# Optimization experiments

Hardware: AMD Instinct MI355X
Metric: run time of the kernel (lower is better)

## Reference

```python
import jax, jax.numpy as jnp
import numpy as np
from functools import partial

ALPHA = 0.1
THETA = 0.5
N_NODES = 100000
N_EDGES = 3200000


def _gcn_norm(edge_index, num_nodes):
    # add self loops, compute symmetric normalization D^-1/2 (A+I) D^-1/2
    loops = jnp.arange(num_nodes, dtype=edge_index.dtype)
    src = jnp.concatenate([edge_index[0], loops])
    dst = jnp.concatenate([edge_index[1], loops])
    deg = jax.ops.segment_sum(jnp.ones_like(dst, dtype=jnp.float32), dst,
                              num_segments=num_nodes)
    dinv = jnp.where(deg > 0, jax.lax.rsqrt(deg), 0.0)
    norm = dinv[src] * dinv[dst]  # [E+N]
    return src, dst, norm


def _propagate(h, src, dst, norm, num_nodes):
    # out[i] = sum_{e: dst[e]=i} norm[e] * h[src[e]]
    msg = h[src] * norm[:, None]
    return jax.ops.segment_sum(msg, dst, num_segments=num_nodes)


def setup_inputs() -> dict:
    key = jax.random.key(0)
    ks = jax.random.split(key, 7)
    H, Fin, Fout, L = 256, 512, 64, 8
    x = jax.random.normal(ks[0], (N_NODES, Fin), dtype=jnp.float32)
    edge_index = jax.random.randint(ks[1], (2, N_EDGES), 0, N_NODES, dtype=jnp.int64)
    s = 1.0 / np.sqrt(Fin)
    W0 = jax.random.normal(ks[2], (Fin, H), dtype=jnp.float32) * s
    b0 = jax.random.normal(ks[3], (H,), dtype=jnp.float32) * 0.01
    Ws = jax.random.normal(ks[4], (L, H, H), dtype=jnp.float32) / np.sqrt(H)
    Wc = jax.random.normal(ks[5], (H, Fout), dtype=jnp.float32) / np.sqrt(H)
    bc = jax.random.normal(ks[6], (Fout,), dtype=jnp.float32) * 0.01
    return {"x": x, "edge_index": edge_index, "W0": W0, "b0": b0,
            "Ws": Ws, "Wc": Wc, "bc": bc}


def reference(x, edge_index, W0, b0, Ws, Wc, bc):
    num_nodes = x.shape[0]
    src, dst, norm = _gcn_norm(edge_index, num_nodes)
    # initial projection (dropout is identity in eval mode)
    x0 = jax.nn.relu(x @ W0 + b0)  # [N, H]
    h = x0
    layer_num = Ws.shape[0]
    for i in range(layer_num):
        beta = float(np.log(THETA / (i + 1) + 1.0))
        agg = _propagate(h, src, dst, norm, num_nodes)          # Ahat @ h
        z = (1.0 - ALPHA) * agg + ALPHA * x0                    # initial residual
        h = jax.nn.relu((1.0 - beta) * z + beta * (z @ Ws[i]))  # identity mapping
    embedding = h
    logits = embedding @ Wc + bc
    soft_label = jax.nn.softmax(logits, axis=1)
    hard_label = jnp.argmax(soft_label, axis=1)
    return logits, embedding, soft_label, hard_label
```

## Files before the change

### kernel.cpp

```cpp
#include <hip/hip_runtime.h>
#include <hip/hip_bf16.h>
#include <math.h>

#define NN   100000
#define FIN  512
#define HH   256
#define FOUT 64

typedef __attribute__((ext_vector_type(8))) short s16x8;
typedef __attribute__((ext_vector_type(4))) float f32x4;

__global__ void k_count(const int* __restrict__ dst, int* __restrict__ cnt, int E) {
    int i = blockIdx.x * 256 + threadIdx.x;
    if (i < E) atomicAdd(&cnt[dst[i]], 1);
}

__global__ void k_block_sums(const int* __restrict__ cnt, int* __restrict__ partial, int n) {
    __shared__ int red[256];
    int base = blockIdx.x * 1024;
    int t = threadIdx.x;
    int s = 0;
#pragma unroll
    for (int i = 0; i < 4; i++) { int idx = base + t * 4 + i; if (idx < n) s += cnt[idx]; }
    red[t] = s; __syncthreads();
    for (int off = 128; off > 0; off >>= 1) {
        if (t < off) red[t] += red[t + off];
        __syncthreads();
    }
    if (t == 0) partial[blockIdx.x] = red[0];
}

__global__ void k_scan_partials(int* partial, int nb, int* row_ptr, int n) {
    if (threadIdx.x == 0) {
        int run = 0;
        for (int i = 0; i < nb; i++) { int v = partial[i]; partial[i] = run; run += v; }
        row_ptr[n] = run;
    }
}

__global__ void k_write_rowptr(const int* __restrict__ cnt, const int* __restrict__ partial,
                               int* __restrict__ row_ptr, int* __restrict__ cur, int n) {
    __shared__ int sc[256];
    int base = blockIdx.x * 1024;
    int t = threadIdx.x;
    int v[4]; int s = 0;
#pragma unroll
    for (int i = 0; i < 4; i++) { int idx = base + t * 4 + i; v[i] = (idx < n) ? cnt[idx] : 0; s += v[i]; }
    sc[t] = s; __syncthreads();
    for (int off = 1; off < 256; off <<= 1) {
        int add = (t >= off) ? sc[t - off] : 0;
        __syncthreads();
        sc[t] += add;
        __syncthreads();
    }
    int run = partial[blockIdx.x] + sc[t] - s;
#pragma unroll
    for (int i = 0; i < 4; i++) {
        int idx = base + t * 4 + i;
        if (idx < n) { row_ptr[idx] = run; cur[idx] = run; run += v[i]; }
    }
}

__global__ void k_dinv(const int* __restrict__ cnt, float* __restrict__ dinv, int n) {
    int i = blockIdx.x * 256 + threadIdx.x;
    if (i < n) dinv[i] = 1.0f / sqrtf((float)(cnt[i] + 1));
}

__global__ void k_scatter(const int* __restrict__ src, const int* __restrict__ dst,
                          const float* __restrict__ dinv, int* __restrict__ cur,
                          int* __restrict__ src_sorted, float* __restrict__ norm_sorted, int E) {
    int i = blockIdx.x * 256 + threadIdx.x;
    if (i < E) {
        int s = src[i], d = dst[i];
        int p = atomicAdd(&cur[d], 1);
        src_sorted[p] = s;
        norm_sorted[p] = dinv[s] * dinv[d];
    }
}

__device__ __forceinline__ short f2bf_rn(float f) {
    unsigned b = __float_as_uint(f);
    unsigned r = b + 0x7FFFu + ((b >> 16) & 1u);
    return (short)(r >> 16);
}
__device__ __forceinline__ float bf2f(short h) {
    return __uint_as_float(((unsigned)(unsigned short)h) << 16);
}
__device__ __forceinline__ void split_bf16(float f, short& hi, short& lo) {
    hi = f2bf_rn(f);
    lo = f2bf_rn(f - bf2f(hi));
}

__global__ void k_wprep(const float* __restrict__ W, short* __restrict__ whi,
                        short* __restrict__ wlo, int K) {
    int t = blockIdx.x * 256 + threadIdx.x;
    int total = K * HH / 8;
    if (t >= total) return;
    int colin = t & 15, g = (t >> 4) & 3, nt = (t >> 6) & 15, kt = t >> 10;
    int col = nt * 16 + colin, kb = kt * 32 + g * 8;
    s16x8 h8, l8;
#pragma unroll
    for (int j = 0; j < 8; j++) {
        float f = W[(size_t)(kb + j) * HH + col];
        short h, l; split_bf16(f, h, l);
        h8[j] = h; l8[j] = l;
    }
    *(s16x8*)&whi[(size_t)t * 8] = h8;
    *(s16x8*)&wlo[(size_t)t * 8] = l8;
}

__global__ __launch_bounds__(256) void k_gemm0(
    const float* __restrict__ A, const short* __restrict__ Whi, const short* __restrict__ Wlo,
    const float* __restrict__ bias, float* __restrict__ C, int M) {
    __shared__ short As_hi[2048];
    __shared__ short As_lo[2048];
    int tid = threadIdx.x, lane = tid & 63, wid = tid >> 6;
    int wm = wid >> 1, wn = wid & 1;
    int bm = blockIdx.x * 64;
    int st_row = tid >> 2, st_g = tid & 3;
    int st_cphys = ((st_row & 15) ^ ((st_g & 1) << 2)) + 16 * st_g + 64 * (st_row >> 4);
    const float* st_ap = A + (size_t)(bm + st_row) * FIN + st_g * 8;
    bool st_ok = (bm + st_row) < M;
    int fr_g = lane >> 4, fr_r = lane & 15;
    int fr_base = (fr_r ^ ((fr_g & 1) << 2)) + 16 * fr_g;
    int c0 = (fr_base + 64 * (wm * 2 + 0)) * 8;
    int c1 = (fr_base + 64 * (wm * 2 + 1)) * 8;
    int lane_off = fr_g * 16 + fr_r;
    f32x4 acc[2][8] = {};
    for (int kt = 0; kt < FIN / 32; kt++) {
        int k0 = kt * 32;
        f32x4 v0 = {0.f, 0.f, 0.f, 0.f}, v1 = {0.f, 0.f, 0.f, 0.f};
        if (st_ok) { v0 = *(const f32x4*)(st_ap + k0); v1 = *(const f32x4*)(st_ap + k0 + 4); }
        s16x8 h8, l8;
        {
            float fv[8] = {v0.x, v0.y, v0.z, v0.w, v1.x, v1.y, v1.z, v1.w};
#pragma unroll
            for (int j = 0; j < 8; j++) { short hh, ll; split_bf16(fv[j], hh, ll); h8[j] = hh; l8[j] = ll; }
        }
        *(s16x8*)&As_hi[st_cphys * 8] = h8;
        *(s16x8*)&As_lo[st_cphys * 8] = l8;
        __syncthreads();
        s16x8 ah0 = *(const s16x8*)&As_hi[c0], al0 = *(const s16x8*)&As_lo[c0];
        s16x8 ah1 = *(const s16x8*)&As_hi[c1], al1 = *(const s16x8*)&As_lo[c1];
        size_t btile = (size_t)kt * 1024 + (size_t)(wn * 8) * 64;
#pragma unroll
        for (int ct = 0; ct < 8; ct++) {
            s16x8 bh = *(const s16x8*)&Whi[(btile + ct * 64 + lane_off) * 8];
            s16x8 bl = *(const s16x8*)&Wlo[(btile + ct * 64 + lane_off) * 8];
            acc[0][ct] = __builtin_amdgcn_mfma_f32_16x16x32_bf16(ah0, bh, acc[0][ct], 0, 0, 0);
            acc[0][ct] = __builtin_amdgcn_mfma_f32_16x16x32_bf16(al0, bh, acc[0][ct], 0, 0, 0);
            acc[0][ct] = __builtin_amdgcn_mfma_f32_16x16x32_bf16(ah0, bl, acc[0][ct], 0, 0, 0);
            acc[1][ct] = __builtin_amdgcn_mfma_f32_16x16x32_bf16(ah1, bh, acc[1][ct], 0, 0, 0);
            acc[1][ct] = __builtin_amdgcn_mfma_f32_16x16x32_bf16(al1, bh, acc[1][ct], 0, 0, 0);
            acc[1][ct] = __builtin_amdgcn_mfma_f32_16x16x32_bf16(ah1, bl, acc[1][ct], 0, 0, 0);
        }
        __syncthreads();
    }
    int rsub = (lane >> 4) * 4, csub = lane & 15;
#pragma unroll
    for (int rt = 0; rt < 2; rt++)
#pragma unroll
        for (int ct = 0; ct < 8; ct++) {
            int col = wn * 128 + ct * 16 + csub;
            int r0 = bm + wm * 32 + rt * 16 + rsub;
#pragma unroll
            for (int reg = 0; reg < 4; reg++) {
                int row = r0 + reg;
                if (row < M) C[(size_t)row * HH + col] = fmaxf(acc[rt][ct][reg] + bias[col], 0.f);
            }
        }
}

__global__ __launch_bounds__(256) void k_layer(
    const float* __restrict__ h, const float* __restrict__ x0,
    const int* __restrict__ row_ptr, const int* __restrict__ src_sorted,
    const float* __restrict__ norm_sorted, const float* __restrict__ dinv,
    const short* __restrict__ Whi, const short* __restrict__ Wlo,
    float* __restrict__ C, int M, float beta) {
    __shared__ float zbuf[16384];
    __shared__ short As_hi[2048];
    __shared__ short As_lo[2048];
    int tid = threadIdx.x, lane = tid & 63, wid = tid >> 6;
    int bm = blockIdx.x * 64;

    {
        int f = lane * 4;
        for (int r16 = 0; r16 < 16; r16++) {
            int rl = r16 * 4 + wid;
            int node = bm + rl;
            if (node < M) {
                size_t base = (size_t)node * HH + f;
                float di = dinv[node];
                float sw = di * di;
                f32x4 acc = *(const f32x4*)&h[base];
                acc *= sw;
                int e = __builtin_amdgcn_readfirstlane(row_ptr[node]);
                int end = __builtin_amdgcn_readfirstlane(row_ptr[node + 1]);
                for (; e + 3 < end; e += 4) {
                    int s0 = src_sorted[e], s1 = src_sorted[e + 1];
                    int s2 = src_sorted[e + 2], s3 = src_sorted[e + 3];
                    float w0 = norm_sorted[e], w1 = norm_sorted[e + 1];
                    float w2 = norm_sorted[e + 2], w3 = norm_sorted[e + 3];
                    f32x4 v0 = *(const f32x4*)&h[(size_t)s0 * HH + f];
                    f32x4 v1 = *(const f32x4*)&h[(size_t)s1 * HH + f];
                    f32x4 v2 = *(const f32x4*)&h[(size_t)s2 * HH + f];
                    f32x4 v3 = *(const f32x4*)&h[(size_t)s3 * HH + f];
                    acc += w0 * v0 + w1 * v1 + w2 * v2 + w3 * v3;
                }
                for (; e < end; e++) {
                    int s0 = src_sorted[e];
                    float w0 = norm_sorted[e];
                    acc += w0 * (*(const f32x4*)&h[(size_t)s0 * HH + f]);
                }
                f32x4 xv = __builtin_nontemporal_load((const f32x4*)&x0[base]);
                f32x4 z = 0.9f * acc + 0.1f * xv;
                int phys = lane ^ (rl & 7);
                *(f32x4*)&zbuf[rl * 256 + phys * 4] = z;
            }
        }
    }
    __syncthreads();

    int wm = wid >> 1, wn = wid & 1;
    int st_row = tid >> 2, st_g = tid & 3;
    int st_cphys = ((st_row & 15) ^ ((st_g & 1) << 2)) + 16 * st_g + 64 * (st_row >> 4);
    int fr_g = lane >> 4, fr_r = lane & 15;
    int fr_base = (fr_r ^ ((fr_g & 1) << 2)) + 16 * fr_g;
    int c0 = (fr_base + 64 * (wm * 2 + 0)) * 8;
    int c1 = (fr_base + 64 * (wm * 2 + 1)) * 8;
    int lane_off = fr_g * 16 + fr_r;
    int zr = st_row * 256, swz = st_row & 7;
    f32x4 acc[2][8] = {};
    for (int kt = 0; kt < 8; kt++) {
        int b0 = kt * 8 + st_g * 2;
        f32x4 v0 = *(const f32x4*)&zbuf[zr + ((b0 ^ swz) * 4)];
        f32x4 v1 = *(const f32x4*)&zbuf[zr + (((b0 + 1) ^ swz) * 4)];
        s16x8 h8, l8;
        {
            float fv[8] = {v0.x, v0.y, v0.z, v0.w, v1.x, v1.y, v1.z, v1.w};
#pragma unroll
            for (int j = 0; j < 8; j++) { short hh, ll; split_bf16(fv[j], hh, ll); h8[j] = hh; l8[j] = ll; }
        }
        *(s16x8*)&As_hi[st_cphys * 8] = h8;
        *(s16x8*)&As_lo[st_cphys * 8] = l8;
        __syncthreads();
        s16x8 ah0 = *(const s16x8*)&As_hi[c0], al0 = *(const s16x8*)&As_lo[c0];
        s16x8 ah1 = *(const s16x8*)&As_hi[c1], al1 = *(const s16x8*)&As_lo[c1];
        size_t btile = (size_t)kt * 1024 + (size_t)(wn * 8) * 64;
#pragma unroll
        for (int ct = 0; ct < 8; ct++) {
            s16x8 bh = *(const s16x8*)&Whi[(btile + ct * 64 + lane_off) * 8];
            s16x8 bl = *(const s16x8*)&Wlo[(btile + ct * 64 + lane_off) * 8];
            acc[0][ct] = __builtin_amdgcn_mfma_f32_16x16x32_bf16(ah0, bh, acc[0][ct], 0, 0, 0);
            acc[0][ct] = __builtin_amdgcn_mfma_f32_16x16x32_bf16(al0, bh, acc[0][ct], 0, 0, 0);
            acc[0][ct] = __builtin_amdgcn_mfma_f32_16x16x32_bf16(ah0, bl, acc[0][ct], 0, 0, 0);
            acc[1][ct] = __builtin_amdgcn_mfma_f32_16x16x32_bf16(ah1, bh, acc[1][ct], 0, 0, 0);
            acc[1][ct] = __builtin_amdgcn_mfma_f32_16x16x32_bf16(al1, bh, acc[1][ct], 0, 0, 0);
            acc[1][ct] = __builtin_amdgcn_mfma_f32_16x16x32_bf16(ah1, bl, acc[1][ct], 0, 0, 0);
        }
        __syncthreads();
    }

    int rsub = (lane >> 4) * 4, csub = lane & 15;
    float ob = 1.f - beta;
#pragma unroll
    for (int rt = 0; rt < 2; rt++)
#pragma unroll
        for (int ct = 0; ct < 8; ct++) {
            int col = wn * 128 + ct * 16 + csub;
            int r0 = wm * 32 + rt * 16 + rsub;
#pragma unroll
            for (int reg = 0; reg < 4; reg++) {
                int rl = r0 + reg;
                int row = bm + rl;
                if (row < M) {
                    float z = zbuf[rl * 256 + (((col >> 2) ^ (rl & 7)) * 4) + (col & 3)];
                    C[(size_t)row * HH + col] = fmaxf(ob * z + beta * acc[rt][ct][reg], 0.f);
                }
            }
        }
}

__global__ __launch_bounds__(256) void k_final(
    const float* __restrict__ h, const float* __restrict__ Wc, const float* __restrict__ bc,
    float* __restrict__ logits, float* __restrict__ soft, float* __restrict__ hard) {
    int wv = threadIdx.x >> 6, lane = threadIdx.x & 63;
    int node = blockIdx.x * 4 + wv;
    if (node >= NN) return;
    const float* hr = &h[(size_t)node * HH];
    float acc = bc[lane];
    for (int k = 0; k < HH; k += 4) {
        f32x4 hv = *(const f32x4*)&hr[k];
        acc += hv.x * Wc[(k + 0) * FOUT + lane];
        acc += hv.y * Wc[(k + 1) * FOUT + lane];
        acc += hv.z * Wc[(k + 2) * FOUT + lane];
        acc += hv.w * Wc[(k + 3) * FOUT + lane];
    }
    float m = acc;
    for (int off = 32; off > 0; off >>= 1) m = fmaxf(m, __shfl_xor(m, off));
    float ev = expf(acc - m);
    float s = ev;
    for (int off = 32; off > 0; off >>= 1) s += __shfl_xor(s, off);
    float sm = ev / s;
    int idx = lane; float v = acc;
    for (int off = 1; off < 64; off <<= 1) {
        float ov = __shfl_xor(v, off);
        int oi = __shfl_xor(idx, off);
        if (ov > v || (ov == v && oi < idx)) { v = ov; idx = oi; }
    }
    logits[(size_t)node * FOUT + lane] = acc;
    soft[(size_t)node * FOUT + lane] = sm;
    if (lane == 0) hard[node] = (float)idx;
}

extern "C" void kernel_launch(void* const* d_in, const int* in_sizes, int n_in,
                              void* d_out, int out_size, void* d_ws, size_t ws_size,
                              hipStream_t stream) {
    const float* x  = (const float*)d_in[0];
    const int*   ei = (const int*)d_in[1];
    const float* W0 = (const float*)d_in[2];
    const float* b0 = (const float*)d_in[3];
    const float* Ws = (const float*)d_in[4];
    const float* Wc = (const float*)d_in[5];
    const float* bc = (const float*)d_in[6];
    const int E = in_sizes[1] / 2;
    const int N = in_sizes[0] / FIN;
    const int L = in_sizes[4] / (HH * HH);

    float* out    = (float*)d_out;
    float* logits = out;
    float* emb    = out + (size_t)N * FOUT;
    float* soft   = emb + (size_t)N * HH;
    float* hard   = soft + (size_t)N * FOUT;

    char* p = (char*)d_ws;
    size_t off = 0;
    auto alloc = [&](size_t bytes) { void* r = p + off; off += (bytes + 255) & ~(size_t)255; return r; };
    int*   cnt         = (int*)alloc((size_t)N * 4);
    int*   row_ptr     = (int*)alloc((size_t)(N + 1) * 4);
    int*   cur         = (int*)alloc((size_t)N * 4);
    int*   partial     = (int*)alloc(4096 * 4);
    float* dinv        = (float*)alloc((size_t)N * 4);
    int*   src_sorted  = (int*)alloc((size_t)E * 4);
    float* norm_sorted = (float*)alloc((size_t)E * 4);
    float* X0          = (float*)alloc((size_t)N * HH * 4);
    float* hA          = (float*)alloc((size_t)N * HH * 4);
    short* W0hi        = (short*)alloc((size_t)FIN * HH * 2);
    short* W0lo        = (short*)alloc((size_t)FIN * HH * 2);
    short* Wshi        = (short*)alloc((size_t)L * HH * HH * 2);
    short* Wslo        = (short*)alloc((size_t)L * HH * HH * 2);

    const int* srcp = ei;
    const int* dstp = ei + E;

    hipMemsetAsync(cnt, 0, (size_t)N * 4, stream);
    k_count<<<(E + 255) / 256, 256, 0, stream>>>(dstp, cnt, E);
    const int nb = (N + 1023) / 1024;
    k_block_sums<<<nb, 256, 0, stream>>>(cnt, partial, N);
    k_scan_partials<<<1, 64, 0, stream>>>(partial, nb, row_ptr, N);
    k_write_rowptr<<<nb, 256, 0, stream>>>(cnt, partial, row_ptr, cur, N);
    k_dinv<<<(N + 255) / 256, 256, 0, stream>>>(cnt, dinv, N);
    k_scatter<<<(E + 255) / 256, 256, 0, stream>>>(srcp, dstp, dinv, cur, src_sorted, norm_sorted, E);

    k_wprep<<<(FIN * HH / 8 + 255) / 256, 256, 0, stream>>>(W0, W0hi, W0lo, FIN);
    for (int i = 0; i < L; i++)
        k_wprep<<<(HH * HH / 8 + 255) / 256, 256, 0, stream>>>(
            Ws + (size_t)i * HH * HH, Wshi + (size_t)i * HH * HH, Wslo + (size_t)i * HH * HH, HH);

    const int nblk = (N + 63) / 64;
    k_gemm0<<<nblk, 256, 0, stream>>>(x, W0hi, W0lo, b0, X0, N);

    const float* hsrc = X0;
    for (int i = 0; i < L; i++) {
        float beta = (float)log(0.5 / (i + 1) + 1.0);
        float* hdst = (i & 1) ? emb : hA;
        if (i == L - 1) hdst = emb;
        k_layer<<<nblk, 256, 0, stream>>>(hsrc, X0, row_ptr, src_sorted, norm_sorted, dinv,
                                          Wshi + (size_t)i * HH * HH, Wslo + (size_t)i * HH * HH,
                                          hdst, N, beta);
        hsrc = hdst;
    }
    k_final<<<(N + 3) / 4, 256, 0, stream>>>(emb, Wc, bc, logits, soft, hard);
}
```

Baseline: 5.660 ms.

## Store hidden features in 64-column chunked layout and split edges across lane groups

Hidden states and X0 are now stored as four column-major chunks of 64 features, each with rows of 256 bytes. The aggregation loop gathers one chunk at a time, so the gathered working set per pass is a quarter of the full array and fits better in cache. Within each wavefront, four lane groups of 16 process interleaved edges in parallel and are combined with cross-lane shuffles. The cost is four passes over the edge list per block, shuffle reductions, and an extra ping-pong buffer, with only the last layer writing row-major output.

```diff
diff --git a/kernel.cpp b/kernel.cpp
--- a/kernel.cpp
+++ b/kernel.cpp
@@ -117,6 +117,7 @@
     int tid = threadIdx.x, lane = tid & 63, wid = tid >> 6;
     int wm = wid >> 1, wn = wid & 1;
     int bm = blockIdx.x * 64;
+    size_t CS = (size_t)M * 64;
     int st_row = tid >> 2, st_g = tid & 3;
     int st_cphys = ((st_row & 15) ^ ((st_g & 1) << 2)) + 16 * st_g + 64 * (st_row >> 4);
     const float* st_ap = A + (size_t)(bm + st_row) * FIN + st_g * 8;
@@ -166,7 +167,10 @@
 #pragma unroll
             for (int reg = 0; reg < 4; reg++) {
                 int row = r0 + reg;
-                if (row < M) C[(size_t)row * HH + col] = fmaxf(acc[rt][ct][reg] + bias[col], 0.f);
+                if (row < M) {
+                    float o = fmaxf(acc[rt][ct][reg] + bias[col], 0.f);
+                    C[(size_t)(col >> 6) * CS + (size_t)row * 64 + (col & 63)] = o;
+                }
             }
         }
 }
@@ -176,46 +180,52 @@
     const int* __restrict__ row_ptr, const int* __restrict__ src_sorted,
     const float* __restrict__ norm_sorted, const float* __restrict__ dinv,
     const short* __restrict__ Whi, const short* __restrict__ Wlo,
-    float* __restrict__ C, int M, float beta) {
+    float* __restrict__ C, int M, float beta, int rowmajor) {
     __shared__ float zbuf[16384];
     __shared__ short As_hi[2048];
     __shared__ short As_lo[2048];
     int tid = threadIdx.x, lane = tid & 63, wid = tid >> 6;
     int bm = blockIdx.x * 64;
-
-    {
-        int f = lane * 4;
+    int f16 = lane & 15, slot = lane >> 4;
+    size_t CS = (size_t)M * 64;
+
+    for (int ch = 0; ch < 4; ch++) {
+        const float* hc  = h  + (size_t)ch * CS;
+        const float* x0c = x0 + (size_t)ch * CS;
         for (int r16 = 0; r16 < 16; r16++) {
             int rl = r16 * 4 + wid;
             int node = bm + rl;
             if (node < M) {
-                size_t base = (size_t)node * HH + f;
-                float di = dinv[node];
-                float sw = di * di;
-                f32x4 acc = *(const f32x4*)&h[base];
-                acc *= sw;
-                int e = __builtin_amdgcn_readfirstlane(row_ptr[node]);
-                int end = __builtin_amdgcn_readfirstlane(row_ptr[node + 1]);
-                for (; e + 3 < end; e += 4) {
-                    int s0 = src_sorted[e], s1 = src_sorted[e + 1];
-                    int s2 = src_sorted[e + 2], s3 = src_sorted[e + 3];
-                    float w0 = norm_sorted[e], w1 = norm_sorted[e + 1];
-                    float w2 = norm_sorted[e + 2], w3 = norm_sorted[e + 3];
-                    f32x4 v0 = *(const f32x4*)&h[(size_t)s0 * HH + f];
-                    f32x4 v1 = *(const f32x4*)&h[(size_t)s1 * HH + f];
-                    f32x4 v2 = *(const f32x4*)&h[(size_t)s2 * HH + f];
-                    f32x4 v3 = *(const f32x4*)&h[(size_t)s3 * HH + f];
-                    acc += w0 * v0 + w1 * v1 + w2 * v2 + w3 * v3;
-                }
-                for (; e < end; e++) {
-                    int s0 = src_sorted[e];
-                    float w0 = norm_sorted[e];
-                    acc += w0 * (*(const f32x4*)&h[(size_t)s0 * HH + f]);
-                }
-                f32x4 xv = __builtin_nontemporal_load((const f32x4*)&x0[base]);
-                f32x4 z = 0.9f * acc + 0.1f * xv;
-                int phys = lane ^ (rl & 7);
-                *(f32x4*)&zbuf[rl * 256 + phys * 4] = z;
+                int e0 = __builtin_amdgcn_readfirstlane(row_ptr[node]);
+                int e1 = __builtin_amdgcn_readfirstlane(row_ptr[node + 1]);
+                f32x4 acc = {0.f, 0.f, 0.f, 0.f};
+                int e = e0 + slot;
+                for (; e + 4 < e1; e += 8) {
+                    int s0 = src_sorted[e];     float w0 = norm_sorted[e];
+                    int s1 = src_sorted[e + 4]; float w1 = norm_sorted[e + 4];
+                    f32x4 v0 = *(const f32x4*)&hc[(size_t)s0 * 64 + f16 * 4];
+                    f32x4 v1 = *(const f32x4*)&hc[(size_t)s1 * 64 + f16 * 4];
+                    acc += w0 * v0 + w1 * v1;
+                }
+                if (e < e1) {
+                    int s0 = src_sorted[e]; float w0 = norm_sorted[e];
+                    acc += w0 * (*(const f32x4*)&hc[(size_t)s0 * 64 + f16 * 4]);
+                }
+#pragma unroll
+                for (int c = 0; c < 4; c++) {
+                    float t = acc[c];
+                    t += __shfl_xor(t, 16);
+                    t += __shfl_xor(t, 32);
+                    acc[c] = t;
+                }
+                if (slot == 0) {
+                    float di = dinv[node], sw = di * di;
+                    f32x4 hrow = *(const f32x4*)&hc[(size_t)node * 64 + f16 * 4];
+                    f32x4 xv   = *(const f32x4*)&x0c[(size_t)node * 64 + f16 * 4];
+                    f32x4 z = 0.9f * (acc + sw * hrow) + 0.1f * xv;
+                    int phys = (ch * 16 + f16) ^ (rl & 7);
+                    *(f32x4*)&zbuf[rl * 256 + phys * 4] = z;
+                }
             }
         }
     }
@@ -275,7 +285,9 @@
                 int row = bm + rl;
                 if (row < M) {
                     float z = zbuf[rl * 256 + (((col >> 2) ^ (rl & 7)) * 4) + (col & 3)];
-                    C[(size_t)row * HH + col] = fmaxf(ob * z + beta * acc[rt][ct][reg], 0.f);
+                    float o = fmaxf(ob * z + beta * acc[rt][ct][reg], 0.f);
+                    if (rowmajor) C[(size_t)row * HH + col] = o;
+                    else C[(size_t)(col >> 6) * CS + (size_t)row * 64 + (col & 63)] = o;
                 }
             }
         }
@@ -343,8 +355,9 @@
     float* dinv        = (float*)alloc((size_t)N * 4);
     int*   src_sorted  = (int*)alloc((size_t)E * 4);
     float* norm_sorted = (float*)alloc((size_t)E * 4);
-    float* X0          = (float*)alloc((size_t)N * HH * 4);
-    float* hA          = (float*)alloc((size_t)N * HH * 4);
+    float* X0c         = (float*)alloc((size_t)N * HH * 4);
+    float* hAc         = (float*)alloc((size_t)N * HH * 4);
+    float* hBc         = (float*)alloc((size_t)N * HH * 4);
     short* W0hi        = (short*)alloc((size_t)FIN * HH * 2);
     short* W0lo        = (short*)alloc((size_t)FIN * HH * 2);
     short* Wshi        = (short*)alloc((size_t)L * HH * HH * 2);
@@ -368,16 +381,16 @@
             Ws + (size_t)i * HH * HH, Wshi + (size_t)i * HH * HH, Wslo + (size_t)i * HH * HH, HH);
 
     const int nblk = (N + 63) / 64;
-    k_gemm0<<<nblk, 256, 0, stream>>>(x, W0hi, W0lo, b0, X0, N);
-
-    const float* hsrc = X0;
+    k_gemm0<<<nblk, 256, 0, stream>>>(x, W0hi, W0lo, b0, X0c, N);
+
+    const float* hsrc = X0c;
     for (int i = 0; i < L; i++) {
         float beta = (float)log(0.5 / (i + 1) + 1.0);
-        float* hdst = (i & 1) ? emb : hA;
-        if (i == L - 1) hdst = emb;
-        k_layer<<<nblk, 256, 0, stream>>>(hsrc, X0, row_ptr, src_sorted, norm_sorted, dinv,
+        int last = (i == L - 1);
+        float* hdst = last ? emb : ((i & 1) ? hBc : hAc);
+        k_layer<<<nblk, 256, 0, stream>>>(hsrc, X0c, row_ptr, src_sorted, norm_sorted, dinv,
                                           Wshi + (size_t)i * HH * HH, Wslo + (size_t)i * HH * HH,
-                                          hdst, N, beta);
+                                          hdst, N, beta, last);
         hsrc = hdst;
     }
     k_final<<<(N + 3) / 4, 256, 0, stream>>>(emb, Wc, bc, logits, soft, hard);
```

After: 9.787 ms. 72.9% more time.
